# Kernel optimization log

Measured on AMD Instinct MI355X. Metric: run time of the kernel, lower is better.

Reference implementation:

```python
import jax, jax.numpy as jnp
import numpy as np

N = 8192      # number of tree nodes
H = 256       # lstm_hiddens
D = 300       # word_dims (in_dim)
V = 50000     # vocab (n_embed)
K = 4         # max children per node (4-ary tree)
OUT = 4       # category_num


def _make_tree():
    # Static 4-ary tree: node i's children are 4i+1..4i+4 (if < N).
    idx = np.arange(N)[:, None] * K + 1 + np.arange(K)[None, :]
    mask = (idx < N).astype(np.float32)
    idx = np.where(idx < N, idx, 0)
    return jnp.asarray(idx, dtype=jnp.int32), jnp.asarray(mask, dtype=jnp.float32)


def setup_inputs() -> dict:
    key = jax.random.key(0)
    ks = jax.random.split(key, 6)
    xs = jax.random.randint(ks[0], (N,), 0, V, dtype=jnp.int32)
    emb_table = jax.random.normal(ks[1], (V, D), jnp.float32) * 0.1
    Wx = jax.random.normal(ks[2], (4, H, D), jnp.float32) * (1.0 / np.sqrt(D))
    bx = jnp.zeros((4, H), jnp.float32)
    Wh = jax.random.normal(ks[3], (4, H, H), jnp.float32) * (1.0 / np.sqrt(H))
    bh = jnp.zeros((4, H), jnp.float32)
    Wout = jax.random.normal(ks[4], (OUT, H), jnp.float32) * (1.0 / np.sqrt(H))
    bout = jnp.zeros((OUT,), jnp.float32)
    child_idx, child_mask = _make_tree()
    return dict(xs=xs, child_idx=child_idx, child_mask=child_mask,
                emb_table=emb_table, Wx=Wx, bx=bx, Wh=Wh, bh=bh,
                Wout=Wout, bout=bout)


def reference(xs, child_idx, child_mask, emb_table, Wx, bx, Wh, bh, Wout, bout):
    # Embedding lookup (dropout is identity in eval)
    X = emb_table[xs]                                   # [N, D]
    # Precompute all x-side gate projections in one batched matmul.
    # Gate order: 0=i, 1=f, 2=o, 3=u  (matches ix/fx/ox/ux).
    gx = jnp.einsum('ghd,nd->ngh', Wx, X) + bx          # [N, 4, H]

    Wh_i, Wh_f, Wh_o, Wh_u = Wh[0], Wh[1], Wh[2], Wh[3]
    bh_i, bh_f, bh_o, bh_u = bh[0], bh[1], bh[2], bh[3]

    def step(carry, i):
        Hbuf, Cbuf = carry
        cidx = child_idx[i]                              # [K]
        m = child_mask[i][:, None]                       # [K, 1]
        Hc = Hbuf[cidx] * m                              # [K, H] masked child h
        Cc = Cbuf[cidx] * m                              # [K, H] masked child c
        hs = Hc.sum(0)                                   # child_h_sum
        g = gx[i]                                        # [4, H]
        ig = jax.nn.sigmoid(g[0] + Wh_i @ hs + bh_i)
        og = jax.nn.sigmoid(g[2] + Wh_o @ hs + bh_o)
        ug = jnp.tanh(g[3] + Wh_u @ hs + bh_u)
        f = jax.nn.sigmoid(g[1] + Hc @ Wh_f.T + bh_f)    # [K, H] per-child forget
        c = ig * ug + (f * Cc).sum(0)                    # masked children have Cc=0
        h = og * jnp.tanh(c)
        return (Hbuf.at[i].set(h), Cbuf.at[i].set(c)), None

    order = jnp.arange(N - 1, -1, -1)                    # children before parents
    init = (jnp.zeros((N, H), X.dtype), jnp.zeros((N, H), X.dtype))
    (Hbuf, _), _ = jax.lax.scan(step, init, order)

    logits = Wout @ Hbuf[0] + bout                       # root output
    return jax.nn.log_softmax(logits)
```

## Files before the change

kernel.cpp:

```cpp
#include <hip/hip_runtime.h>


#define N_NODES 8192
#define HDIM 256
#define DDIM 300
#define GXC 1024
#define LEAF_FIRST 2048
#define WH_STRIDE 65536

__device__ __forceinline__ float sigf(float x) { return 1.0f / (1.0f + __expf(-x)); }

__global__ __launch_bounds__(256) void gx_gemm(
    const int* __restrict__ xs, const float* __restrict__ emb,
    const float* __restrict__ Wx, const float* __restrict__ bx,
    float* __restrict__ gx)
{
    const int lid  = blockIdx.x + blockIdx.y * gridDim.x;
    const int rowt = (lid & 7) + ((lid >> 3) & 15) * 8;
    const int colt = lid >> 7;
    const int n0 = rowt * 64;
    const int c0 = colt * 64;
    if (n0 >= LEAF_FIRST && c0 >= 256 && c0 < 512) return;

    __shared__ __align__(16) float As[16][68];
    __shared__ __align__(16) float Bs[16][68];
    const int tid  = threadIdx.x;
    const int sr   = tid >> 2;
    const int sk   = (tid & 3) << 2;
    const int trow = (tid >> 4) << 2;
    const int tcol = (tid & 15) << 2;

    const long arow = (long)xs[n0 + sr] * DDIM;
    const long brow = (long)(c0 + sr) * DDIM;

    float acc[4][4] = {};

    float4 av = make_float4(0.f, 0.f, 0.f, 0.f);
    float4 bv = make_float4(0.f, 0.f, 0.f, 0.f);
    if (sk < DDIM) {
        av = *(const float4*)(emb + arow + sk);
        bv = *(const float4*)(Wx  + brow + sk);
    }

    for (int k0 = 0; k0 < DDIM; k0 += 16) {
        __syncthreads();
        As[sk+0][sr] = av.x; As[sk+1][sr] = av.y; As[sk+2][sr] = av.z; As[sk+3][sr] = av.w;
        Bs[sk+0][sr] = bv.x; Bs[sk+1][sr] = bv.y; Bs[sk+2][sr] = bv.z; Bs[sk+3][sr] = bv.w;
        __syncthreads();

        const int kn = k0 + 16;
        av = make_float4(0.f, 0.f, 0.f, 0.f);
        bv = make_float4(0.f, 0.f, 0.f, 0.f);
        if (kn + sk < DDIM) {
            av = *(const float4*)(emb + arow + kn + sk);
            bv = *(const float4*)(Wx  + brow + kn + sk);
        }

        #pragma unroll
        for (int k = 0; k < 16; k++) {
            float4 a = *(const float4*)&As[k][trow];
            float4 b = *(const float4*)&Bs[k][tcol];
            float avv[4] = {a.x, a.y, a.z, a.w};
            float bvv[4] = {b.x, b.y, b.z, b.w};
            #pragma unroll
            for (int i = 0; i < 4; i++)
                #pragma unroll
                for (int j = 0; j < 4; j++)
                    acc[i][j] = fmaf(avv[i], bvv[j], acc[i][j]);
        }
    }

    #pragma unroll
    for (int i = 0; i < 4; i++) {
        const int col = c0 + tcol;
        float4 r;
        r.x = acc[i][0] + bx[col + 0];
        r.y = acc[i][1] + bx[col + 1];
        r.z = acc[i][2] + bx[col + 2];
        r.w = acc[i][3] + bx[col + 3];
        *(float4*)(gx + (long)(n0 + trow + i) * GXC + col) = r;
    }
}

__global__ __launch_bounds__(256) void leaf_kernel(
    const float* __restrict__ gx, const float* __restrict__ bh,
    float* __restrict__ Hb, float* __restrict__ Cb)
{
    const int t = threadIdx.x;
    const float bi = bh[t], bo = bh[512 + t], bu = bh[768 + t];
    #pragma unroll
    for (int s = 0; s < 4; s++) {
        const int node = LEAF_FIRST + blockIdx.x * 4 + s;
        const float* g = gx + (long)node * GXC;
        const float gi = g[t]       + bi;
        const float go = g[512 + t] + bo;
        const float gu = g[768 + t] + bu;
        const float c  = sigf(gi) * tanhf(gu);
        const float h  = sigf(go) * tanhf(c);
        Hb[(long)node * HDIM + t] = h;
        Cb[(long)node * HDIM + t] = c;
    }
}

__global__ __launch_bounds__(256) void level_gemm(
    int first, int M, const float* __restrict__ Hb,
    const int* __restrict__ child_idx, const float* __restrict__ child_mask,
    const float* __restrict__ Wh, float* __restrict__ D)
{
    __shared__ __align__(16) float Xs[16][68];
    __shared__ __align__(16) float Ws[16][68];
    const int tid  = threadIdx.x;
    const int sec  = blockIdx.y;
    const int c0   = blockIdx.x * 64;
    const int r0   = blockIdx.z * 64;
    const int sr   = tid >> 2;
    const int sk   = (tid & 3) << 2;
    const int trow = (tid >> 4) << 2;
    const int tcol = (tid & 15) << 2;

    const float* Wg;
    if      (sec == 0) Wg = Wh;
    else if (sec == 1) Wg = Wh + 2 * WH_STRIDE;
    else if (sec == 2) Wg = Wh + 3 * WH_STRIDE;
    else               Wg = Wh + 1 * WH_STRIDE;

    const int  nl    = c0 + sr;
    const bool valid = nl < M;
    int   ci[4];
    float cm[4] = {0.f, 0.f, 0.f, 0.f};
    if (valid) {
        const int n = first + nl;
        if (sec < 3) {
            #pragma unroll
            for (int k = 0; k < 4; k++) {
                ci[k] = child_idx[n * 4 + k];
                cm[k] = child_mask[n * 4 + k];
            }
        } else {
            ci[0] = child_idx[n * 4 + (sec - 3)];
            cm[0] = child_mask[n * 4 + (sec - 3)];
        }
    }
    const long wrow = (long)(r0 + sr) * HDIM;

    float acc[4][4] = {};

    float4 hvr[4], wvr;

    {
        #pragma unroll
        for (int k = 0; k < 4; k++) hvr[k] = make_float4(0.f, 0.f, 0.f, 0.f);
        if (valid) {
            if (sec < 3) {
                #pragma unroll
                for (int k = 0; k < 4; k++)
                    if (cm[k] != 0.f)
                        hvr[k] = *(const float4*)(Hb + ci[k] * HDIM + sk);
            } else if (cm[0] != 0.f) {
                hvr[0] = *(const float4*)(Hb + ci[0] * HDIM + sk);
            }
        }
        wvr = *(const float4*)(Wg + wrow + sk);
    }

    for (int k0 = 0; k0 < HDIM; k0 += 16) {
        __syncthreads();
        float4 xv;
        xv.x = hvr[0].x + hvr[1].x + hvr[2].x + hvr[3].x;
        xv.y = hvr[0].y + hvr[1].y + hvr[2].y + hvr[3].y;
        xv.z = hvr[0].z + hvr[1].z + hvr[2].z + hvr[3].z;
        xv.w = hvr[0].w + hvr[1].w + hvr[2].w + hvr[3].w;
        Xs[sk+0][sr] = xv.x; Xs[sk+1][sr] = xv.y; Xs[sk+2][sr] = xv.z; Xs[sk+3][sr] = xv.w;
        Ws[sk+0][sr] = wvr.x; Ws[sk+1][sr] = wvr.y; Ws[sk+2][sr] = wvr.z; Ws[sk+3][sr] = wvr.w;
        __syncthreads();

        const int kn = k0 + 16;
        if (kn < HDIM) {
            #pragma unroll
            for (int k = 0; k < 4; k++) hvr[k] = make_float4(0.f, 0.f, 0.f, 0.f);
            if (valid) {
                if (sec < 3) {
                    #pragma unroll
                    for (int k = 0; k < 4; k++)
                        if (cm[k] != 0.f)
                            hvr[k] = *(const float4*)(Hb + ci[k] * HDIM + kn + sk);
                } else if (cm[0] != 0.f) {
                    hvr[0] = *(const float4*)(Hb + ci[0] * HDIM + kn + sk);
                }
            }
            wvr = *(const float4*)(Wg + wrow + kn + sk);
        }

        #pragma unroll
        for (int k = 0; k < 16; k++) {
            float4 a = *(const float4*)&Ws[k][trow];
            float4 b = *(const float4*)&Xs[k][tcol];
            float avv[4] = {a.x, a.y, a.z, a.w};
            float bvv[4] = {b.x, b.y, b.z, b.w};
            #pragma unroll
            for (int i = 0; i < 4; i++)
                #pragma unroll
                for (int j = 0; j < 4; j++)
                    acc[i][j] = fmaf(avv[i], bvv[j], acc[i][j]);
        }
    }

    #pragma unroll
    for (int j = 0; j < 4; j++) {
        const int col = c0 + tcol + j;
        if (col < M) {
            float4 r;
            r.x = acc[0][j]; r.y = acc[1][j]; r.z = acc[2][j]; r.w = acc[3][j];
            *(float4*)(D + ((long)(sec * M + col)) * HDIM + r0 + trow) = r;
        }
    }
}

__global__ __launch_bounds__(256) void level_pointwise(
    int first, int M, int do_out,
    const float* __restrict__ gx, const float* __restrict__ D,
    const int* __restrict__ child_idx, const float* __restrict__ child_mask,
    const float* __restrict__ bh, float* __restrict__ Hb, float* __restrict__ Cb,
    const float* __restrict__ Wout, const float* __restrict__ bout,
    float* __restrict__ out)
{
    __shared__ float hroot[HDIM];
    __shared__ float logits[4];
    const int nl = blockIdx.x;
    const int n  = first + nl;
    const int t  = threadIdx.x;
    const float di  = D[((long)(0 * M + nl)) * HDIM + t];
    const float dO  = D[((long)(1 * M + nl)) * HDIM + t];
    const float du  = D[((long)(2 * M + nl)) * HDIM + t];
    const float* g = gx + (long)n * GXC;
    const float gi  = g[t]       + bh[t]       + di;
    const float gfb = g[256 + t] + bh[256 + t];
    const float go  = g[512 + t] + bh[512 + t] + dO;
    const float gu  = g[768 + t] + bh[768 + t] + du;

    float c = sigf(gi) * tanhf(gu);
    #pragma unroll
    for (int k = 0; k < 4; k++) {
        const float m = child_mask[n * 4 + k];
        if (m != 0.f) {
            const float df = D[((long)((3 + k) * M + nl)) * HDIM + t];
            const float cc = Cb[(long)child_idx[n * 4 + k] * HDIM + t];
            c = fmaf(sigf(gfb + df), cc, c);
        }
    }
    const float h = sigf(go) * tanhf(c);
    Hb[(long)n * HDIM + t] = h;
    Cb[(long)n * HDIM + t] = c;

    if (do_out) {
        hroot[t] = h;
        __syncthreads();
        const int o    = t >> 6;
        const int lane = t & 63;
        float s = 0.f;
        for (int jj = lane; jj < HDIM; jj += 64)
            s = fmaf(Wout[o * HDIM + jj], hroot[jj], s);
        #pragma unroll
        for (int off = 32; off > 0; off >>= 1)
            s += __shfl_down(s, off, 64);
        if (lane == 0) logits[o] = s + bout[o];
        __syncthreads();
        if (t == 0) {
            float m = logits[0];
            #pragma unroll
            for (int i = 1; i < 4; i++) m = fmaxf(m, logits[i]);
            float se = 0.f;
            #pragma unroll
            for (int i = 0; i < 4; i++) se += __expf(logits[i] - m);
            const float lse = m + __logf(se);
            #pragma unroll
            for (int i = 0; i < 4; i++) out[i] = logits[i] - lse;
        }
    }
}

extern "C" void kernel_launch(void* const* d_in, const int* in_sizes, int n_in,
                              void* d_out, int out_size, void* d_ws, size_t ws_size,
                              hipStream_t stream)
{
    const int*   xs         = (const int*)  d_in[0];
    const int*   child_idx  = (const int*)  d_in[1];
    const float* child_mask = (const float*)d_in[2];
    const float* emb        = (const float*)d_in[3];
    const float* Wx         = (const float*)d_in[4];
    const float* bx         = (const float*)d_in[5];
    const float* Wh         = (const float*)d_in[6];
    const float* bh         = (const float*)d_in[7];
    const float* Wout       = (const float*)d_in[8];
    const float* bout       = (const float*)d_in[9];
    float* out = (float*)d_out;

    float* gxb = (float*)d_ws;
    float* Hb  = gxb + (size_t)N_NODES * GXC;
    float* Cb  = Hb  + (size_t)N_NODES * HDIM;
    float* Dbuf = gxb + (size_t)LEAF_FIRST * GXC;

    gx_gemm<<<dim3(GXC / 64, N_NODES / 64), 256, 0, stream>>>(xs, emb, Wx, bx, gxb);
    leaf_kernel<<<(N_NODES - LEAF_FIRST) / 4, 256, 0, stream>>>(gxb, bh, Hb, Cb);

    const int pf[7] = {1365, 341, 85, 21, 5, 1, 0};
    const int pc[7] = { 683, 1024, 256, 64, 16, 4, 1};
    for (int p = 0; p < 7; p++) {
        const int M = pc[p];
        dim3 grid((M + 63) / 64, 7, 4);
        level_gemm<<<grid, 256, 0, stream>>>(pf[p], M, Hb, child_idx, child_mask,
                                             Wh, Dbuf);
        level_pointwise<<<M, 256, 0, stream>>>(pf[p], M, (p == 6) ? 1 : 0,
                                               gxb, Dbuf, child_idx, child_mask,
                                               bh, Hb, Cb, Wout, bout, out);
    }
}
```

Baseline: 322.7 us.

## Fuse recurrent gate GEMM and pointwise update for large tree levels

Adds a level_fused2 kernel for the three widest internal tree levels. For each group of 4 nodes it gathers the child h vectors into shared memory, computes the i/o/u gate projections of the child-h sum and the per-child forget-gate projections, then applies the LSTM cell update in the same kernel. This removes the separate pointwise launch and the round trip of gate pre-activations through global memory for those levels. The cost is that every block re-streams its 64-row slices of the four Wh matrices, so total weight traffic through L2 grows a lot compared with the 64-node tiled GEMM. The gx GEMM also drops a redundant bounds check on its first load.

Result: slower. 407.3 us (+26.2%).

```diff
diff --git a/kernel.cpp b/kernel.cpp
--- a/kernel.cpp
+++ b/kernel.cpp
@@ -7,6 +7,9 @@
 #define GXC 1024
 #define LEAF_FIRST 2048
 #define WH_STRIDE 65536
+#define NG 4
+#define KC 32
+#define WP 66
 
 __device__ __forceinline__ float sigf(float x) { return 1.0f / (1.0f + __expf(-x)); }
 
@@ -35,12 +38,8 @@
 
     float acc[4][4] = {};
 
-    float4 av = make_float4(0.f, 0.f, 0.f, 0.f);
-    float4 bv = make_float4(0.f, 0.f, 0.f, 0.f);
-    if (sk < DDIM) {
-        av = *(const float4*)(emb + arow + sk);
-        bv = *(const float4*)(Wx  + brow + sk);
-    }
+    float4 av = *(const float4*)(emb + arow + sk);
+    float4 bv = *(const float4*)(Wx  + brow + sk);
 
     for (int k0 = 0; k0 < DDIM; k0 += 16) {
         __syncthreads();
@@ -102,6 +101,154 @@
     }
 }
 
+__global__ __launch_bounds__(256) void level_fused2(
+    int first, int M,
+    const float* __restrict__ gx, const int* __restrict__ child_idx,
+    const float* __restrict__ child_mask, const float* __restrict__ Wh,
+    const float* __restrict__ bh, float* __restrict__ Hb, float* __restrict__ Cb)
+{
+    __shared__ __align__(16) float Xh[NG][HDIM];
+    __shared__ __align__(16) float Xc[NG][4][HDIM];
+    __shared__ __align__(16) float Ws[4][KC][WP];
+    __shared__ float Ds[NG][7][64];
+
+    const int t   = threadIdx.x;
+    const int ng0 = blockIdx.x * NG;
+
+    {
+        const int sg   = t >> 6;
+        const int sch  = (t >> 4) & 3;
+        const int sk16 = (t & 15) << 4;
+        const int nl = ng0 + sg;
+        float m = 0.f; long crow = 0;
+        if (nl < M) {
+            const int n = first + nl;
+            crow = (long)child_idx[n * 4 + sch] * HDIM;
+            m    = child_mask[n * 4 + sch];
+        }
+        float4 v[4];
+        #pragma unroll
+        for (int i = 0; i < 4; i++) v[i] = make_float4(0.f, 0.f, 0.f, 0.f);
+        if (m != 0.f) {
+            #pragma unroll
+            for (int i = 0; i < 4; i++)
+                v[i] = *(const float4*)(Hb + crow + sk16 + i * 4);
+        }
+        #pragma unroll
+        for (int i = 0; i < 4; i++)
+            *(float4*)&Xc[sg][sch][sk16 + i * 4] = v[i];
+    }
+    __syncthreads();
+    for (int idx = t; idx < NG * HDIM; idx += 256) {
+        const int g = idx >> 8, k = idx & 255;
+        Xh[g][k] = Xc[g][0][k] + Xc[g][1][k] + Xc[g][2][k] + Xc[g][3][k];
+    }
+
+    const float* Wg[4] = { Wh,
+                           Wh + 2 * WH_STRIDE,
+                           Wh + 3 * WH_STRIDE,
+                           Wh + 1 * WH_STRIDE };
+    const int q   = t >> 2;
+    const int j   = t & 3;
+    const int gi4 = t >> 6;
+    const int r8  = (t & 63) >> 3;
+    const int ks  = t & 7;
+
+    const int rb = blockIdx.y;
+
+    float acc[NG][7];
+    #pragma unroll
+    for (int g = 0; g < NG; g++)
+        #pragma unroll
+        for (int s = 0; s < 7; s++) acc[g][s] = 0.f;
+
+    for (int kc = 0; kc < HDIM / KC; kc++) {
+        __syncthreads();
+        {
+            const float* wb = Wg[gi4] + (long)(rb * 64) * HDIM + kc * KC + ks * 4;
+            #pragma unroll
+            for (int rr = 0; rr < 8; rr++) {
+                const int row = rr * 8 + r8;
+                const float4 wv = *(const float4*)(wb + (long)row * HDIM);
+                Ws[gi4][ks * 4 + 0][row] = wv.x;
+                Ws[gi4][ks * 4 + 1][row] = wv.y;
+                Ws[gi4][ks * 4 + 2][row] = wv.z;
+                Ws[gi4][ks * 4 + 3][row] = wv.w;
+            }
+        }
+        __syncthreads();
+        #pragma unroll
+        for (int kk4 = 0; kk4 < 2; kk4++) {
+            const int kb = j * 8 + kk4 * 4;
+            const int kg = kc * KC + kb;
+            float w0[4], w1[4], w2[4], w3[4];
+            #pragma unroll
+            for (int i = 0; i < 4; i++) {
+                w0[i] = Ws[0][kb + i][q];
+                w1[i] = Ws[1][kb + i][q];
+                w2[i] = Ws[2][kb + i][q];
+                w3[i] = Ws[3][kb + i][q];
+            }
+            #pragma unroll
+            for (int g = 0; g < NG; g++) {
+                const float4 hs = *(const float4*)&Xh[g][kg];
+                const float hv[4] = {hs.x, hs.y, hs.z, hs.w};
+                #pragma unroll
+                for (int i = 0; i < 4; i++) {
+                    acc[g][0] = fmaf(w0[i], hv[i], acc[g][0]);
+                    acc[g][1] = fmaf(w1[i], hv[i], acc[g][1]);
+                    acc[g][2] = fmaf(w2[i], hv[i], acc[g][2]);
+                }
+                #pragma unroll
+                for (int ch = 0; ch < 4; ch++) {
+                    const float4 cv = *(const float4*)&Xc[g][ch][kg];
+                    const float cvv[4] = {cv.x, cv.y, cv.z, cv.w};
+                    #pragma unroll
+                    for (int i = 0; i < 4; i++)
+                        acc[g][3 + ch] = fmaf(w3[i], cvv[i], acc[g][3 + ch]);
+                }
+            }
+        }
+    }
+
+    #pragma unroll
+    for (int g = 0; g < NG; g++)
+        #pragma unroll
+        for (int s = 0; s < 7; s++) {
+            float v = acc[g][s];
+            v += __shfl_xor(v, 1, 64);
+            v += __shfl_xor(v, 2, 64);
+            if (j == 0) Ds[g][s][q] = v;
+        }
+    __syncthreads();
+
+    {
+        const int pg = t >> 6, r = t & 63;
+        const int nl = ng0 + pg;
+        if (nl < M) {
+            const int n    = first + nl;
+            const int grow = rb * 64 + r;
+            const float* gg = gx + (long)n * GXC;
+            const float gi  = gg[grow]       + bh[grow]       + Ds[pg][0][r];
+            const float gfb = gg[256 + grow] + bh[256 + grow];
+            const float go  = gg[512 + grow] + bh[512 + grow] + Ds[pg][1][r];
+            const float gu  = gg[768 + grow] + bh[768 + grow] + Ds[pg][2][r];
+            float c = sigf(gi) * tanhf(gu);
+            #pragma unroll
+            for (int ch = 0; ch < 4; ch++) {
+                const float m = child_mask[n * 4 + ch];
+                if (m != 0.f) {
+                    const long crow = (long)child_idx[n * 4 + ch] * HDIM;
+                    c = fmaf(sigf(gfb + Ds[pg][3 + ch][r]), Cb[crow + grow], c);
+                }
+            }
+            const float h = sigf(go) * tanhf(c);
+            Hb[(long)n * HDIM + grow] = h;
+            Cb[(long)n * HDIM + grow] = c;
+        }
+    }
+}
+
 __global__ __launch_bounds__(256) void level_gemm(
     int first, int M, const float* __restrict__ Hb,
     const int* __restrict__ child_idx, const float* __restrict__ child_mask,
@@ -146,7 +293,6 @@
     float acc[4][4] = {};
 
     float4 hvr[4], wvr;
-
     {
         #pragma unroll
         for (int k = 0; k < 4; k++) hvr[k] = make_float4(0.f, 0.f, 0.f, 0.f);
@@ -303,14 +449,23 @@
     gx_gemm<<<dim3(GXC / 64, N_NODES / 64), 256, 0, stream>>>(xs, emb, Wx, bx, gxb);
     leaf_kernel<<<(N_NODES - LEAF_FIRST) / 4, 256, 0, stream>>>(gxb, bh, Hb, Cb);
 
-    const int pf[7] = {1365, 341, 85, 21, 5, 1, 0};
-    const int pc[7] = { 683, 1024, 256, 64, 16, 4, 1};
-    for (int p = 0; p < 7; p++) {
-        const int M = pc[p];
+    const int pfb[3] = {1365, 341, 85};
+    const int pcb[3] = { 683, 1024, 256};
+    for (int p = 0; p < 3; p++) {
+        const int M = pcb[p];
+        dim3 grid((M + NG - 1) / NG, 4);
+        level_fused2<<<grid, 256, 0, stream>>>(pfb[p], M, gxb, child_idx,
+                                               child_mask, Wh, bh, Hb, Cb);
+    }
+
+    const int pft[4] = {21, 5, 1, 0};
+    const int pct[4] = {64, 16, 4, 1};
+    for (int p = 0; p < 4; p++) {
+        const int M = pct[p];
         dim3 grid((M + 63) / 64, 7, 4);
-        level_gemm<<<grid, 256, 0, stream>>>(pf[p], M, Hb, child_idx, child_mask,
+        level_gemm<<<grid, 256, 0, stream>>>(pft[p], M, Hb, child_idx, child_mask,
                                              Wh, Dbuf);
-        level_pointwise<<<M, 256, 0, stream>>>(pf[p], M, (p == 6) ? 1 : 0,
+        level_pointwise<<<M, 256, 0, stream>>>(pft[p], M, (p == 3) ? 1 : 0,
                                                gxb, Dbuf, child_idx, child_mask,
                                                bh, Hb, Cb, Wout, bout, out);
     }
```

## Fuse tail-level gemm and pointwise via last-block atomic; enlarge gx_gemm tiles

Applied to the files above, without the earlier changes.

For the four smallest tree levels, the separate gemm and pointwise launches become one tail_gemm kernel. Its last finishing block, found with an atomic counter, runs the pointwise LSTM update and the root output, which cuts launch count and the gaps between launches. The gx projection GEMM also moves from 64x64 tiles with 4x4 per-thread microtiles to 128x128 tiles with 8x8 microtiles to raise arithmetic intensity. Risks are lower occupancy from the larger register tiles, counters kept in spare workspace that gx_gemm resets, and the serial single-block pointwise work in the tail.

After: 560.7 us. 73.8% more time.

```diff
diff --git a/kernel.cpp b/kernel.cpp
--- a/kernel.cpp
+++ b/kernel.cpp
@@ -7,78 +7,94 @@
 #define GXC 1024
 #define LEAF_FIRST 2048
 #define WH_STRIDE 65536
+#define TAIL_NBLK 28
 
 __device__ __forceinline__ float sigf(float x) { return 1.0f / (1.0f + __expf(-x)); }
 
 __global__ __launch_bounds__(256) void gx_gemm(
     const int* __restrict__ xs, const float* __restrict__ emb,
     const float* __restrict__ Wx, const float* __restrict__ bx,
-    float* __restrict__ gx)
-{
+    float* __restrict__ gx, unsigned* __restrict__ cnts)
+{
+    if (blockIdx.x == 0 && blockIdx.y == 0 && threadIdx.x == 0) {
+        cnts[0] = 0u; cnts[1] = 0u; cnts[2] = 0u; cnts[3] = 0u;
+    }
+
     const int lid  = blockIdx.x + blockIdx.y * gridDim.x;
-    const int rowt = (lid & 7) + ((lid >> 3) & 15) * 8;
-    const int colt = lid >> 7;
-    const int n0 = rowt * 64;
-    const int c0 = colt * 64;
-    if (n0 >= LEAF_FIRST && c0 >= 256 && c0 < 512) return;
-
-    __shared__ __align__(16) float As[16][68];
-    __shared__ __align__(16) float Bs[16][68];
+    const int rowt = (lid & 7) * 8 + ((lid >> 3) & 7);
+    const int colt = lid >> 6;
+    const int n0 = rowt * 128;
+    const int c0 = colt * 128;
+    if (n0 >= LEAF_FIRST && (colt == 2 || colt == 3)) return;
+
+    __shared__ __align__(16) float As[16][132];
+    __shared__ __align__(16) float Bs[16][132];
     const int tid  = threadIdx.x;
-    const int sr   = tid >> 2;
-    const int sk   = (tid & 3) << 2;
-    const int trow = (tid >> 4) << 2;
-    const int tcol = (tid & 15) << 2;
+    const int sr   = tid >> 1;
+    const int sk8  = (tid & 1) << 3;
+    const int trow = (tid >> 4) << 3;
+    const int tcol = (tid & 15) << 3;
 
     const long arow = (long)xs[n0 + sr] * DDIM;
     const long brow = (long)(c0 + sr) * DDIM;
 
-    float acc[4][4] = {};
-
-    float4 av = make_float4(0.f, 0.f, 0.f, 0.f);
-    float4 bv = make_float4(0.f, 0.f, 0.f, 0.f);
-    if (sk < DDIM) {
-        av = *(const float4*)(emb + arow + sk);
-        bv = *(const float4*)(Wx  + brow + sk);
-    }
+    float acc[8][8] = {};
+
+    float4 a0 = *(const float4*)(emb + arow + sk8);
+    float4 a1 = *(const float4*)(emb + arow + sk8 + 4);
+    float4 b0 = *(const float4*)(Wx  + brow + sk8);
+    float4 b1 = *(const float4*)(Wx  + brow + sk8 + 4);
 
     for (int k0 = 0; k0 < DDIM; k0 += 16) {
         __syncthreads();
-        As[sk+0][sr] = av.x; As[sk+1][sr] = av.y; As[sk+2][sr] = av.z; As[sk+3][sr] = av.w;
-        Bs[sk+0][sr] = bv.x; Bs[sk+1][sr] = bv.y; Bs[sk+2][sr] = bv.z; Bs[sk+3][sr] = bv.w;
+        As[sk8+0][sr] = a0.x; As[sk8+1][sr] = a0.y; As[sk8+2][sr] = a0.z; As[sk8+3][sr] = a0.w;
+        As[sk8+4][sr] = a1.x; As[sk8+5][sr] = a1.y; As[sk8+6][sr] = a1.z; As[sk8+7][sr] = a1.w;
+        Bs[sk8+0][sr] = b0.x; Bs[sk8+1][sr] = b0.y; Bs[sk8+2][sr] = b0.z; Bs[sk8+3][sr] = b0.w;
+        Bs[sk8+4][sr] = b1.x; Bs[sk8+5][sr] = b1.y; Bs[sk8+6][sr] = b1.z; Bs[sk8+7][sr] = b1.w;
         __syncthreads();
 
         const int kn = k0 + 16;
-        av = make_float4(0.f, 0.f, 0.f, 0.f);
-        bv = make_float4(0.f, 0.f, 0.f, 0.f);
-        if (kn + sk < DDIM) {
-            av = *(const float4*)(emb + arow + kn + sk);
-            bv = *(const float4*)(Wx  + brow + kn + sk);
+        a0 = make_float4(0.f,0.f,0.f,0.f); a1 = a0; b0 = a0; b1 = a0;
+        if (kn < DDIM) {
+            if (kn + sk8 < DDIM) {
+                a0 = *(const float4*)(emb + arow + kn + sk8);
+                b0 = *(const float4*)(Wx  + brow + kn + sk8);
+            }
+            if (kn + sk8 + 4 < DDIM) {
+                a1 = *(const float4*)(emb + arow + kn + sk8 + 4);
+                b1 = *(const float4*)(Wx  + brow + kn + sk8 + 4);
+            }
         }
 
         #pragma unroll
         for (int k = 0; k < 16; k++) {
-            float4 a = *(const float4*)&As[k][trow];
-            float4 b = *(const float4*)&Bs[k][tcol];
-            float avv[4] = {a.x, a.y, a.z, a.w};
-            float bvv[4] = {b.x, b.y, b.z, b.w};
-            #pragma unroll
-            for (int i = 0; i < 4; i++)
+            const float4 av0 = *(const float4*)&As[k][trow];
+            const float4 av1 = *(const float4*)&As[k][trow + 4];
+            const float4 bv0 = *(const float4*)&Bs[k][tcol];
+            const float4 bv1 = *(const float4*)&Bs[k][tcol + 4];
+            const float aa[8] = {av0.x,av0.y,av0.z,av0.w,av1.x,av1.y,av1.z,av1.w};
+            const float bb[8] = {bv0.x,bv0.y,bv0.z,bv0.w,bv1.x,bv1.y,bv1.z,bv1.w};
+            #pragma unroll
+            for (int i = 0; i < 8; i++)
                 #pragma unroll
-                for (int j = 0; j < 4; j++)
-                    acc[i][j] = fmaf(avv[i], bvv[j], acc[i][j]);
-        }
-    }
-
-    #pragma unroll
-    for (int i = 0; i < 4; i++) {
-        const int col = c0 + tcol;
-        float4 r;
-        r.x = acc[i][0] + bx[col + 0];
-        r.y = acc[i][1] + bx[col + 1];
-        r.z = acc[i][2] + bx[col + 2];
-        r.w = acc[i][3] + bx[col + 3];
-        *(float4*)(gx + (long)(n0 + trow + i) * GXC + col) = r;
+                for (int j = 0; j < 8; j++)
+                    acc[i][j] = fmaf(aa[i], bb[j], acc[i][j]);
+        }
+    }
+
+    const int col = c0 + tcol;
+    const float4 bxa = *(const float4*)(bx + col);
+    const float4 bxb = *(const float4*)(bx + col + 4);
+    #pragma unroll
+    for (int i = 0; i < 8; i++) {
+        float4 r0, r1;
+        r0.x = acc[i][0] + bxa.x; r0.y = acc[i][1] + bxa.y;
+        r0.z = acc[i][2] + bxa.z; r0.w = acc[i][3] + bxa.w;
+        r1.x = acc[i][4] + bxb.x; r1.y = acc[i][5] + bxb.y;
+        r1.z = acc[i][6] + bxb.z; r1.w = acc[i][7] + bxb.w;
+        float* dst = gx + (long)(n0 + trow + i) * GXC + col;
+        *(float4*)dst = r0;
+        *(float4*)(dst + 4) = r1;
     }
 }
 
@@ -102,17 +118,13 @@
     }
 }
 
-__global__ __launch_bounds__(256) void level_gemm(
-    int first, int M, const float* __restrict__ Hb,
-    const int* __restrict__ child_idx, const float* __restrict__ child_mask,
-    const float* __restrict__ Wh, float* __restrict__ D)
-{
-    __shared__ __align__(16) float Xs[16][68];
-    __shared__ __align__(16) float Ws[16][68];
+__device__ __forceinline__ void gemm_body(
+    int first, int M, int sec, int c0, int r0,
+    const float* __restrict__ Hb, const int* __restrict__ child_idx,
+    const float* __restrict__ child_mask, const float* __restrict__ Wh,
+    float* __restrict__ D, float (*Xs)[68], float (*Ws)[68])
+{
     const int tid  = threadIdx.x;
-    const int sec  = blockIdx.y;
-    const int c0   = blockIdx.x * 64;
-    const int r0   = blockIdx.z * 64;
     const int sr   = tid >> 2;
     const int sk   = (tid & 3) << 2;
     const int trow = (tid >> 4) << 2;
@@ -144,24 +156,21 @@
     const long wrow = (long)(r0 + sr) * HDIM;
 
     float acc[4][4] = {};
-
     float4 hvr[4], wvr;
 
-    {
-        #pragma unroll
-        for (int k = 0; k < 4; k++) hvr[k] = make_float4(0.f, 0.f, 0.f, 0.f);
-        if (valid) {
-            if (sec < 3) {
-                #pragma unroll
-                for (int k = 0; k < 4; k++)
-                    if (cm[k] != 0.f)
-                        hvr[k] = *(const float4*)(Hb + ci[k] * HDIM + sk);
-            } else if (cm[0] != 0.f) {
-                hvr[0] = *(const float4*)(Hb + ci[0] * HDIM + sk);
-            }
-        }
-        wvr = *(const float4*)(Wg + wrow + sk);
-    }
+    #pragma unroll
+    for (int k = 0; k < 4; k++) hvr[k] = make_float4(0.f, 0.f, 0.f, 0.f);
+    if (valid) {
+        if (sec < 3) {
+            #pragma unroll
+            for (int k = 0; k < 4; k++)
+                if (cm[k] != 0.f)
+                    hvr[k] = *(const float4*)(Hb + ci[k] * HDIM + sk);
+        } else if (cm[0] != 0.f) {
+            hvr[0] = *(const float4*)(Hb + ci[0] * HDIM + sk);
+        }
+    }
+    wvr = *(const float4*)(Wg + wrow + sk);
 
     for (int k0 = 0; k0 < HDIM; k0 += 16) {
         __syncthreads();
@@ -216,16 +225,22 @@
     }
 }
 
+__global__ __launch_bounds__(256) void level_gemm(
+    int first, int M, const float* __restrict__ Hb,
+    const int* __restrict__ child_idx, const float* __restrict__ child_mask,
+    const float* __restrict__ Wh, float* __restrict__ D)
+{
+    __shared__ __align__(16) float Xs[16][68];
+    __shared__ __align__(16) float Ws[16][68];
+    gemm_body(first, M, blockIdx.y, blockIdx.x * 64, blockIdx.z * 64,
+              Hb, child_idx, child_mask, Wh, D, Xs, Ws);
+}
+
 __global__ __launch_bounds__(256) void level_pointwise(
-    int first, int M, int do_out,
-    const float* __restrict__ gx, const float* __restrict__ D,
+    int first, int M, const float* __restrict__ gx, const float* __restrict__ D,
     const int* __restrict__ child_idx, const float* __restrict__ child_mask,
-    const float* __restrict__ bh, float* __restrict__ Hb, float* __restrict__ Cb,
-    const float* __restrict__ Wout, const float* __restrict__ bout,
-    float* __restrict__ out)
-{
-    __shared__ float hroot[HDIM];
-    __shared__ float logits[4];
+    const float* __restrict__ bh, float* __restrict__ Hb, float* __restrict__ Cb)
+{
     const int nl = blockIdx.x;
     const int n  = first + nl;
     const int t  = threadIdx.x;
@@ -251,9 +266,63 @@
     const float h = sigf(go) * tanhf(c);
     Hb[(long)n * HDIM + t] = h;
     Cb[(long)n * HDIM + t] = c;
+}
+
+__global__ __launch_bounds__(256) void tail_gemm(
+    int first, int M, int do_out,
+    const float* __restrict__ Hb_in, const int* __restrict__ child_idx,
+    const float* __restrict__ child_mask, const float* __restrict__ Wh,
+    float* __restrict__ D, const float* __restrict__ gx,
+    const float* __restrict__ bh, float* __restrict__ Hb, float* __restrict__ Cb,
+    const float* __restrict__ Wout, const float* __restrict__ bout,
+    float* __restrict__ out, unsigned* __restrict__ cnt)
+{
+    __shared__ __align__(16) float Xs[16][68];
+    __shared__ __align__(16) float Ws[16][68];
+    __shared__ unsigned is_last;
+    __shared__ float hroot[HDIM];
+    __shared__ float logits[4];
+
+    gemm_body(first, M, blockIdx.y, blockIdx.x * 64, blockIdx.z * 64,
+              Hb_in, child_idx, child_mask, Wh, D, Xs, Ws);
+
+    __threadfence();
+    if (threadIdx.x == 0)
+        is_last = (atomicAdd(cnt, 1u) == TAIL_NBLK - 1u) ? 1u : 0u;
+    __syncthreads();
+    if (!is_last) return;
+    __threadfence();
+
+    const int t = threadIdx.x;
+    for (int idx = t; idx < M * HDIM; idx += 256) {
+        const int nl = idx >> 8;
+        const int r  = idx & 255;
+        const int n  = first + nl;
+        const float di  = D[((long)(0 * M + nl)) * HDIM + r];
+        const float dO  = D[((long)(1 * M + nl)) * HDIM + r];
+        const float du  = D[((long)(2 * M + nl)) * HDIM + r];
+        const float* g = gx + (long)n * GXC;
+        const float gi  = g[r]       + bh[r]       + di;
+        const float gfb = g[256 + r] + bh[256 + r];
+        const float go  = g[512 + r] + bh[512 + r] + dO;
+        const float gu  = g[768 + r] + bh[768 + r] + du;
+        float c = sigf(gi) * tanhf(gu);
+        #pragma unroll
+        for (int k = 0; k < 4; k++) {
+            const float m = child_mask[n * 4 + k];
+            if (m != 0.f) {
+                const float df = D[((long)((3 + k) * M + nl)) * HDIM + r];
+                const float cc = Cb[(long)child_idx[n * 4 + k] * HDIM + r];
+                c = fmaf(sigf(gfb + df), cc, c);
+            }
+        }
+        const float h = sigf(go) * tanhf(c);
+        Hb[(long)n * HDIM + r] = h;
+        Cb[(long)n * HDIM + r] = c;
+        if (do_out) hroot[r] = h;
+    }
 
     if (do_out) {
-        hroot[t] = h;
         __syncthreads();
         const int o    = t >> 6;
         const int lane = t & 63;
@@ -299,19 +368,29 @@
     float* Hb  = gxb + (size_t)N_NODES * GXC;
     float* Cb  = Hb  + (size_t)N_NODES * HDIM;
     float* Dbuf = gxb + (size_t)LEAF_FIRST * GXC;
-
-    gx_gemm<<<dim3(GXC / 64, N_NODES / 64), 256, 0, stream>>>(xs, emb, Wx, bx, gxb);
+    unsigned* cnts = (unsigned*)(gxb + (size_t)(N_NODES - 1) * GXC + 256);
+
+    gx_gemm<<<dim3(8, 64), 256, 0, stream>>>(xs, emb, Wx, bx, gxb, cnts);
     leaf_kernel<<<(N_NODES - LEAF_FIRST) / 4, 256, 0, stream>>>(gxb, bh, Hb, Cb);
 
-    const int pf[7] = {1365, 341, 85, 21, 5, 1, 0};
-    const int pc[7] = { 683, 1024, 256, 64, 16, 4, 1};
-    for (int p = 0; p < 7; p++) {
-        const int M = pc[p];
+    const int pfb[3] = {1365, 341, 85};
+    const int pcb[3] = { 683, 1024, 256};
+    for (int p = 0; p < 3; p++) {
+        const int M = pcb[p];
         dim3 grid((M + 63) / 64, 7, 4);
-        level_gemm<<<grid, 256, 0, stream>>>(pf[p], M, Hb, child_idx, child_mask,
+        level_gemm<<<grid, 256, 0, stream>>>(pfb[p], M, Hb, child_idx, child_mask,
                                              Wh, Dbuf);
-        level_pointwise<<<M, 256, 0, stream>>>(pf[p], M, (p == 6) ? 1 : 0,
-                                               gxb, Dbuf, child_idx, child_mask,
-                                               bh, Hb, Cb, Wout, bout, out);
-    }
-}
+        level_pointwise<<<M, 256, 0, stream>>>(pfb[p], M, gxb, Dbuf, child_idx,
+                                               child_mask, bh, Hb, Cb);
+    }
+
+    const int pft[4] = {21, 5, 1, 0};
+    const int pct[4] = {64, 16, 4, 1};
+    for (int p = 0; p < 4; p++) {
+        dim3 grid(1, 7, 4);
+        tail_gemm<<<grid, 256, 0, stream>>>(pft[p], pct[p], (p == 3) ? 1 : 0,
+                                            Hb, child_idx, child_mask, Wh, Dbuf,
+                                            gxb, bh, Hb, Cb, Wout, bout, out,
+                                            cnts + p);
+    }
+}
```
